# Kernel optimization log

Hardware: AMD Instinct MI355X
Metric: run time of the kernel (lower is better)

The kernel has to match this reference:

```python
import jax, jax.numpy as jnp
import numpy as np

B, C, H, W = 8, 512, 96, 96
CQ = C // 8


def setup_inputs() -> dict:
    key = jax.random.key(0)
    ks = jax.random.split(key, 8)
    s = 1.0 / np.sqrt(C)  # conv-like init scale to keep logits sane
    return {
        "x": jax.random.normal(ks[0], (B, C, H, W), jnp.float32),
        "Wq": jax.random.normal(ks[1], (CQ, C), jnp.float32) * s,
        "bq": jax.random.normal(ks[2], (CQ,), jnp.float32) * s,
        "Wk": jax.random.normal(ks[3], (CQ, C), jnp.float32) * s,
        "bk": jax.random.normal(ks[4], (CQ,), jnp.float32) * s,
        "Wv": jax.random.normal(ks[5], (C, C), jnp.float32) * s,
        "bv": jax.random.normal(ks[6], (C,), jnp.float32) * s,
        "gamma": jax.random.normal(ks[7], (1,), jnp.float32),
    }


def reference(x, Wq, bq, Wk, bk, Wv, bv, gamma):
    # 1x1 convs == per-pixel linear projections
    q = jnp.einsum('bchw,oc->bohw', x, Wq) + bq[None, :, None, None]  # [B,CQ,H,W]
    k = jnp.einsum('bchw,oc->bohw', x, Wk) + bk[None, :, None, None]  # [B,CQ,H,W]
    v = jnp.einsum('bchw,oc->bohw', x, Wv) + bv[None, :, None, None]  # [B,C ,H,W]

    h = x.shape[2]
    # column (vertical) attention logits: query at (h,w) vs keys at (j,w)
    energy_H = jnp.einsum('bchw,bcjw->bhwj', q, k)  # [B,H,W,H]
    # row (horizontal) attention logits: query at (h,w) vs keys at (h,j)
    energy_W = jnp.einsum('bchw,bchj->bhwj', q, k)  # [B,H,W,W]

    att = jax.nn.softmax(jnp.concatenate([energy_H, energy_W], axis=-1), axis=-1)
    att_H = att[..., :h]   # [B,H,W,H]
    att_W = att[..., h:]   # [B,H,W,W]

    out_H = jnp.einsum('bcjw,bhwj->bchw', v, att_H)
    out_W = jnp.einsum('bchj,bhwj->bchw', v, att_W)
    return gamma[0] * (out_H + out_W)
```

## Files before the change

### kernel.cpp

```cpp
#include <hip/hip_runtime.h>

#define B 8
#define C 512
#define H 96
#define W 96
#define HW (H*W)
#define KD 512
#define NSP 9216

typedef __attribute__((ext_vector_type(8))) short bf16x8;
typedef __attribute__((ext_vector_type(4))) short short4v;
typedef __attribute__((ext_vector_type(4))) float f32x4;
typedef __attribute__((ext_vector_type(8))) _Float16 f16x8;
typedef __attribute__((ext_vector_type(4))) _Float16 f16x4v;

static __device__ __forceinline__ unsigned short f2bf(float f) {
    unsigned u = __float_as_uint(f);
    return (unsigned short)((u + 0x7FFFu + ((u >> 16) & 1u)) >> 16);
}
static __device__ __forceinline__ float bf2f(unsigned short h) {
    return __uint_as_float(((unsigned)h) << 16);
}
static __device__ __forceinline__ int tidx(int row, int kgrp) {
    return row * 32 + ((kgrp ^ ((row >> 2) & 3)) << 3);
}
static __device__ __forceinline__ int tidx64(int row, int gr) {
    return row * 64 + ((gr ^ (row & 7)) << 3);
}

__global__ __launch_bounds__(256) void split_w(
    const float* __restrict__ Wv, const float* __restrict__ Wq, const float* __restrict__ Wk,
    _Float16* __restrict__ Wv_h,
    unsigned short* __restrict__ Wqk_hi, unsigned short* __restrict__ Wqk_lo)
{
    int i = blockIdx.x * 256 + threadIdx.x;
    if (i < C * C) {
        Wv_h[i] = (_Float16)Wv[i];
    }
    if (i < 128 * C) {
        int m = i / C, k = i % C;
        float f = (m < 64) ? Wq[m * C + k] : Wk[(m - 64) * C + k];
        unsigned short h = f2bf(f);
        Wqk_hi[i] = h;
        Wqk_lo[i] = f2bf(f - bf2f(h));
    }
}

__global__ __launch_bounds__(256, 2) void gemm_v_f16(
    const float* __restrict__ x,
    const _Float16* __restrict__ Wh,
    const float* __restrict__ bias,
    _Float16* __restrict__ out16)
{
    __shared__ _Float16 smem[12288];
    const int X_HI = 0, X_LO = 4096, W_H = 8192;

    int tid = threadIdx.x;
    int n0 = blockIdx.x * 128;
    int m0 = blockIdx.y * 128;
    int b  = blockIdx.z;

    int lane = tid & 63, wave = tid >> 6;
    int wr = wave >> 1, wc = wave & 1;
    int l15 = lane & 15, l4 = lane >> 4;

    int tn = tid & 31, tk = tid >> 5;
    int nloc = tn * 4, kloc = tk * 4;
    const float* xp = x + ((size_t)b * KD + kloc) * NSP + n0 + nloc;
    int kg = tk >> 1, khalf = tk & 1;

    int wrow0 = tid >> 2, wkg0 = tid & 3;
    int wrow1 = (tid + 256) >> 2, wkg1 = (tid + 256) & 3;
    const _Float16* wp0 = Wh + (size_t)(m0 + wrow0) * KD + wkg0 * 8;
    const _Float16* wp1 = Wh + (size_t)(m0 + wrow1) * KD + wkg1 * 8;

    f32x4 acc[4][4];
    #pragma unroll
    for (int i = 0; i < 4; ++i)
        #pragma unroll
        for (int j = 0; j < 4; ++j)
            acc[i][j] = (f32x4){0.f, 0.f, 0.f, 0.f};

    float4 t4[4];
    f16x8 wv0, wv1;
    #pragma unroll
    for (int kk = 0; kk < 4; ++kk) t4[kk] = *(const float4*)(xp + (size_t)kk * NSP);
    wv0 = *(const f16x8*)wp0;
    wv1 = *(const f16x8*)wp1;

    for (int k0 = 0; k0 < KD; k0 += 32) {
        float4 t4n[4];
        f16x8 wv0n, wv1n;
        if (k0 + 32 < KD) {
            #pragma unroll
            for (int kk = 0; kk < 4; ++kk)
                t4n[kk] = *(const float4*)(xp + (size_t)(k0 + 32 + kk) * NSP);
            wv0n = *(const f16x8*)(wp0 + k0 + 32);
            wv1n = *(const f16x8*)(wp1 + k0 + 32);
        }
        #pragma unroll
        for (int nn = 0; nn < 4; ++nn) {
            int n = nloc + nn;
            f16x4v hi, lo;
            #pragma unroll
            for (int kk = 0; kk < 4; ++kk) {
                float f = ((const float*)&t4[kk])[nn];
                _Float16 hh = (_Float16)f;
                hi[kk] = hh;
                lo[kk] = (_Float16)(f - (float)hh);
            }
            int base = tidx(n, kg) + khalf * 4;
            *(f16x4v*)&smem[X_HI + base] = hi;
            *(f16x4v*)&smem[X_LO + base] = lo;
        }
        *(f16x8*)&smem[W_H + tidx(wrow0, wkg0)] = wv0;
        *(f16x8*)&smem[W_H + tidx(wrow1, wkg1)] = wv1;
        __syncthreads();

        f16x8 af[4], bh_[4], bl_[4];
        #pragma unroll
        for (int f = 0; f < 4; ++f) {
            int ra = wr * 64 + f * 16 + l15;
            int rb = wc * 64 + f * 16 + l15;
            af[f]  = *(const f16x8*)&smem[W_H  + tidx(ra, l4)];
            bh_[f] = *(const f16x8*)&smem[X_HI + tidx(rb, l4)];
        }
        #pragma unroll
        for (int i = 0; i < 4; ++i)
            #pragma unroll
            for (int j = 0; j < 4; ++j)
                acc[i][j] = __builtin_amdgcn_mfma_f32_16x16x32_f16(af[i], bh_[j], acc[i][j], 0, 0, 0);
        #pragma unroll
        for (int f = 0; f < 4; ++f) {
            int rb = wc * 64 + f * 16 + l15;
            bl_[f] = *(const f16x8*)&smem[X_LO + tidx(rb, l4)];
        }
        #pragma unroll
        for (int i = 0; i < 4; ++i)
            #pragma unroll
            for (int j = 0; j < 4; ++j)
                acc[i][j] = __builtin_amdgcn_mfma_f32_16x16x32_f16(af[i], bl_[j], acc[i][j], 0, 0, 0);
        __syncthreads();

        #pragma unroll
        for (int kk = 0; kk < 4; ++kk) t4[kk] = t4n[kk];
        wv0 = wv0n; wv1 = wv1n;
    }

    #pragma unroll
    for (int i = 0; i < 4; ++i) {
        #pragma unroll
        for (int r = 0; r < 4; ++r) {
            int row = m0 + wr * 64 + i * 16 + l4 * 4 + r;
            float bv = bias[row];
            #pragma unroll
            for (int j = 0; j < 4; ++j) {
                int col = n0 + wc * 64 + j * 16 + l15;
                out16[((size_t)b * C + row) * NSP + col] = (_Float16)(acc[i][j][r] + bv);
            }
        }
    }
}

__global__ __launch_bounds__(256, 2) void gemm_qk_bf16(
    const float* __restrict__ x,
    const unsigned short* __restrict__ Wh,
    const unsigned short* __restrict__ Wl,
    const float* __restrict__ bias0,
    const float* __restrict__ bias1,
    unsigned short* __restrict__ qh, unsigned short* __restrict__ ql,
    unsigned short* __restrict__ kh, unsigned short* __restrict__ kl)
{
    __shared__ short smem[16384];
    const int X_HI = 0, X_LO = 4096, W_HI = 8192, W_LO = 12288;

    int tid = threadIdx.x;
    int n0 = blockIdx.x * 128;
    int b  = blockIdx.z;

    int lane = tid & 63, wave = tid >> 6;
    int wr = wave >> 1, wc = wave & 1;
    int l15 = lane & 15, l4 = lane >> 4;

    int tn = tid & 31, tk = tid >> 5;
    int nloc = tn * 4, kloc = tk * 4;
    const float* xp = x + ((size_t)b * KD + kloc) * NSP + n0 + nloc;
    int kg = tk >> 1, khalf = tk & 1;

    int wrow[4], wkg[4];
    const unsigned short* wp[4];
    #pragma unroll
    for (int it = 0; it < 4; ++it) {
        int gi = tid + it * 256;
        int sel = gi >> 9;
        int t = gi & 511;
        wrow[it] = t >> 2; wkg[it] = t & 3;
        wp[it] = (sel ? Wl : Wh) + (size_t)wrow[it] * KD + wkg[it] * 8;
    }
    int wdst[4];
    #pragma unroll
    for (int it = 0; it < 4; ++it)
        wdst[it] = ((tid + it * 256) >> 9 ? W_LO : W_HI) + tidx(wrow[it], wkg[it]);

    f32x4 acc[4][4];
    #pragma unroll
    for (int i = 0; i < 4; ++i)
        #pragma unroll
        for (int j = 0; j < 4; ++j)
            acc[i][j] = (f32x4){0.f, 0.f, 0.f, 0.f};

    float4 t4[4];
    bf16x8 wv[4];
    #pragma unroll
    for (int kk = 0; kk < 4; ++kk) t4[kk] = *(const float4*)(xp + (size_t)kk * NSP);
    #pragma unroll
    for (int it = 0; it < 4; ++it) wv[it] = *(const bf16x8*)wp[it];

    for (int k0 = 0; k0 < KD; k0 += 32) {
        float4 t4n[4];
        bf16x8 wvn[4];
        if (k0 + 32 < KD) {
            #pragma unroll
            for (int kk = 0; kk < 4; ++kk)
                t4n[kk] = *(const float4*)(xp + (size_t)(k0 + 32 + kk) * NSP);
            #pragma unroll
            for (int it = 0; it < 4; ++it)
                wvn[it] = *(const bf16x8*)(wp[it] + k0 + 32);
        }
        #pragma unroll
        for (int nn = 0; nn < 4; ++nn) {
            int n = nloc + nn;
            short4v hi, lo;
            #pragma unroll
            for (int kk = 0; kk < 4; ++kk) {
                float f = ((const float*)&t4[kk])[nn];
                unsigned short h = f2bf(f);
                hi[kk] = (short)h;
                lo[kk] = (short)f2bf(f - bf2f(h));
            }
            int base = tidx(n, kg) + khalf * 4;
            *(short4v*)&smem[X_HI + base] = hi;
            *(short4v*)&smem[X_LO + base] = lo;
        }
        #pragma unroll
        for (int it = 0; it < 4; ++it)
            *(bf16x8*)&smem[wdst[it]] = wv[it];
        __syncthreads();

        bf16x8 af[4], bf_[4], bl_[4];
        #pragma unroll
        for (int f = 0; f < 4; ++f) {
            int ra = wr * 64 + f * 16 + l15;
            int rb = wc * 64 + f * 16 + l15;
            af[f]  = *(const bf16x8*)&smem[X_HI + tidx(ra, l4)];
            bf_[f] = *(const bf16x8*)&smem[W_HI + tidx(rb, l4)];
        }
        #pragma unroll
        for (int i = 0; i < 4; ++i)
            #pragma unroll
            for (int j = 0; j < 4; ++j)
                acc[i][j] = __builtin_amdgcn_mfma_f32_16x16x32_bf16(af[i], bf_[j], acc[i][j], 0, 0, 0);
        #pragma unroll
        for (int f = 0; f < 4; ++f) {
            int rb = wc * 64 + f * 16 + l15;
            bl_[f] = *(const bf16x8*)&smem[W_LO + tidx(rb, l4)];
        }
        #pragma unroll
        for (int i = 0; i < 4; ++i)
            #pragma unroll
            for (int j = 0; j < 4; ++j)
                acc[i][j] = __builtin_amdgcn_mfma_f32_16x16x32_bf16(af[i], bl_[j], acc[i][j], 0, 0, 0);
        #pragma unroll
        for (int f = 0; f < 4; ++f) {
            int ra = wr * 64 + f * 16 + l15;
            af[f] = *(const bf16x8*)&smem[X_LO + tidx(ra, l4)];
        }
        #pragma unroll
        for (int i = 0; i < 4; ++i)
            #pragma unroll
            for (int j = 0; j < 4; ++j)
                acc[i][j] = __builtin_amdgcn_mfma_f32_16x16x32_bf16(af[i], bf_[j], acc[i][j], 0, 0, 0);
        __syncthreads();

        #pragma unroll
        for (int kk = 0; kk < 4; ++kk) t4[kk] = t4n[kk];
        #pragma unroll
        for (int it = 0; it < 4; ++it) wv[it] = wvn[it];
    }

    #pragma unroll
    for (int i = 0; i < 4; ++i) {
        #pragma unroll
        for (int r = 0; r < 4; ++r) {
            int sp = n0 + wr * 64 + i * 16 + l4 * 4 + r;
            #pragma unroll
            for (int j = 0; j < 4; ++j) {
                int wcol = wc * 64 + j * 16 + l15;
                float val = acc[i][j][r] + (wcol < 64 ? bias0[wcol] : bias1[wcol - 64]);
                unsigned short hi = f2bf(val);
                unsigned short lo = f2bf(val - bf2f(hi));
                size_t off = ((size_t)b * NSP + sp) * 64 + (wcol & 63);
                if (wcol < 64) { qh[off] = hi; ql[off] = lo; }
                else           { kh[off] = hi; kl[off] = lo; }
            }
        }
    }
}

__global__ __launch_bounds__(256, 2) void energy_mfma(
    const unsigned short* __restrict__ qh, const unsigned short* __restrict__ ql,
    const unsigned short* __restrict__ kh, const unsigned short* __restrict__ kl,
    float* __restrict__ out, int pMul, int rMul)
{
    __shared__ short sm[4 * 96 * 64];
    const int T_QH = 0, T_QL = 6144, T_KH = 12288, T_KL = 18432;
    int p = blockIdx.x, b = blockIdx.y;
    int tid = threadIdx.x;
    size_t base = ((size_t)b * HW + (size_t)p * pMul) * 64;
    size_t rstride = (size_t)rMul * 64;

    #pragma unroll
    for (int tile = 0; tile < 4; ++tile) {
        const unsigned short* src = (tile == 0) ? qh : (tile == 1) ? ql : (tile == 2) ? kh : kl;
        int tb = tile * 6144;
        #pragma unroll
        for (int sub = 0; sub < 3; ++sub) {
            int s = sub * 256 + tid;
            int row = s >> 3, g = s & 7;
            bf16x8 d = *(const bf16x8*)&src[base + row * rstride + g * 8];
            *(bf16x8*)&sm[tb + tidx64(row, g)] = d;
        }
    }
    __syncthreads();

    int lane = tid & 63, wave = tid >> 6;
    int wr = wave >> 1, wc = wave & 1;
    int l15 = lane & 15, l4 = lane >> 4;

    f32x4 acc[3][3];
    #pragma unroll
    for (int i = 0; i < 3; ++i)
        #pragma unroll
        for (int j = 0; j < 3; ++j)
            acc[i][j] = (f32x4){0.f, 0.f, 0.f, 0.f};

    #pragma unroll
    for (int ks = 0; ks < 2; ++ks) {
        bf16x8 Ah[3], Al[3], Bh[3], Bl[3];
        int gr = ks * 4 + l4;
        #pragma unroll
        for (int i = 0; i < 3; ++i) {
            int ra = wr * 48 + i * 16 + l15;
            int sa = tidx64(ra, gr);
            Ah[i] = *(const bf16x8*)&sm[T_QH + sa];
            Al[i] = *(const bf16x8*)&sm[T_QL + sa];
            int rb = wc * 48 + i * 16 + l15;
            int sb = tidx64(rb, gr);
            Bh[i] = *(const bf16x8*)&sm[T_KH + sb];
            Bl[i] = *(const bf16x8*)&sm[T_KL + sb];
        }
        #pragma unroll
        for (int i = 0; i < 3; ++i)
            #pragma unroll
            for (int j = 0; j < 3; ++j) {
                acc[i][j] = __builtin_amdgcn_mfma_f32_16x16x32_bf16(Ah[i], Bh[j], acc[i][j], 0, 0, 0);
                acc[i][j] = __builtin_amdgcn_mfma_f32_16x16x32_bf16(Ah[i], Bl[j], acc[i][j], 0, 0, 0);
                acc[i][j] = __builtin_amdgcn_mfma_f32_16x16x32_bf16(Al[i], Bh[j], acc[i][j], 0, 0, 0);
            }
    }

    size_t ob = (size_t)(b * 96 + p) * 9216;
    #pragma unroll
    for (int i = 0; i < 3; ++i)
        #pragma unroll
        for (int r = 0; r < 4; ++r) {
            int row = wr * 48 + i * 16 + l4 * 4 + r;
            #pragma unroll
            for (int j = 0; j < 3; ++j) {
                int col = wc * 48 + j * 16 + l15;
                out[ob + (size_t)row * 96 + col] = acc[i][j][r];
            }
        }
}

__global__ __launch_bounds__(256) void maxsum(
    const float* __restrict__ EW, const float* __restrict__ EH,
    const float* __restrict__ gamma, float* __restrict__ ms)
{
    int gw = (blockIdx.x * 256 + threadIdx.x) >> 6;
    int lane = threadIdx.x & 63;
    int b = gw / HW, hw = gw % HW;
    int h = hw / 96, w = hw % 96;
    const float* ew = &EW[((size_t)(b * 96 + h) * 96 + w) * 96];
    const float* eh = &EH[((size_t)(b * 96 + w) * 96 + h) * 96];
    float v0 = ew[lane];
    float v1 = (lane < 32) ? ew[64 + lane] : eh[lane - 32];
    float v2 = eh[32 + lane];
    float m = fmaxf(fmaxf(v0, v1), v2);
    #pragma unroll
    for (int s = 32; s; s >>= 1) m = fmaxf(m, __shfl_xor(m, s));
    float pp = __expf(v0 - m) + __expf(v1 - m) + __expf(v2 - m);
    #pragma unroll
    for (int s = 32; s; s >>= 1) pp += __shfl_xor(pp, s);
    if (lane == 0) {
        ms[(size_t)gw * 2]     = m;
        ms[(size_t)gw * 2 + 1] = gamma[0] / pp;
    }
}

template<int OUT16>
__global__ __launch_bounds__(256) void agg_mfma(
    const float* __restrict__ E, const float* __restrict__ ms,
    const _Float16* __restrict__ v16,
    float* __restrict__ dstF, _Float16* __restrict__ dstH, int msMode)
{
    __shared__ _Float16 satt[3][96 * 32];

    int r  = blockIdx.x;
    int b  = blockIdx.y;
    int tid = threadIdx.x;
    int lane = tid & 63, wave = tid >> 6;
    int l15 = lane & 15, l4 = lane >> 4;

    const float* Eb = &E[(size_t)(b * 96 + r) * 9216];
    int msBase = b * HW;
    #pragma unroll
    for (int it = 0; it < 5; ++it) {
        int g_id = tid + it * 256;
        if (g_id < 1152) {
            int s = g_id / 12, gj = g_id % 12;
            int mi = msMode ? (msBase + s * 96 + r) : (msBase + r * 96 + s);
            float m  = ms[(size_t)mi * 2];
            float sc = ms[(size_t)mi * 2 + 1];
            float4 e0 = *(const float4*)&Eb[s * 96 + gj * 8];
            float4 e1 = *(const float4*)&Eb[s * 96 + gj * 8 + 4];
            float pv[8] = {e0.x, e0.y, e0.z, e0.w, e1.x, e1.y, e1.z, e1.w};
            f16x8 ph;
            #pragma unroll
            for (int u = 0; u < 8; ++u)
                ph[u] = (_Float16)(__expf(pv[u] - m) * sc);
            *(f16x8*)&satt[gj >> 2][tidx(s, gj & 3)] = ph;
        }
    }
    __syncthreads();

    const _Float16* vb = v16 + (size_t)b * C * 9216 + r * 96;

    for (int cc = 0; cc < 4; ++cc) {
        int cbase = cc * 128 + wave * 32;

        f32x4 acc[2][6];
        #pragma unroll
        for (int i = 0; i < 2; ++i)
            #pragma unroll
            for (int n = 0; n < 6; ++n)
                acc[i][n] = (f32x4){0.f, 0.f, 0.f, 0.f};

        #pragma unroll
        for (int kc = 0; kc < 3; ++kc) {
            f16x8 af[2];
            #pragma unroll
            for (int i = 0; i < 2; ++i)
                af[i] = *(const f16x8*)&vb[(size_t)(cbase + i * 16 + l15) * 9216 + kc * 32 + l4 * 8];
            f16x8 Bp[6];
            #pragma unroll
            for (int n = 0; n < 6; ++n)
                Bp[n] = *(const f16x8*)&satt[kc][tidx(n * 16 + l15, l4)];
            #pragma unroll
            for (int i = 0; i < 2; ++i)
                #pragma unroll
                for (int n = 0; n < 6; ++n)
                    acc[i][n] = __builtin_amdgcn_mfma_f32_16x16x32_f16(af[i], Bp[n], acc[i][n], 0, 0, 0);
        }

        #pragma unroll
        for (int i = 0; i < 2; ++i)
            #pragma unroll
            for (int r4 = 0; r4 < 4; ++r4) {
                int cl = cbase + i * 16 + l4 * 4 + r4;
                size_t rowb = ((size_t)b * C + cl) * 9216 + r * 96;
                #pragma unroll
                for (int n = 0; n < 6; ++n) {
                    int s = n * 16 + l15;
                    if (OUT16) dstH[rowb + s] = (_Float16)acc[i][n][r4];
                    else       dstF[rowb + s] = acc[i][n][r4];
                }
            }
    }
}

__global__ __launch_bounds__(256) void transpose_f16(
    const _Float16* __restrict__ src, _Float16* __restrict__ dst)
{
    size_t base = (size_t)blockIdx.x * (96 * 96);
    __shared__ _Float16 t[96][97];
    int tid = threadIdx.x;
    for (int i = tid; i < 96 * 96; i += 256) t[i / 96][i % 96] = src[base + i];
    __syncthreads();
    for (int i = tid; i < 96 * 96; i += 256) dst[base + i] = t[i % 96][i / 96];
}

__global__ __launch_bounds__(256) void transpose_add(
    const _Float16* __restrict__ srcT, float* __restrict__ out)
{
    size_t base = (size_t)blockIdx.x * (96 * 96);
    __shared__ _Float16 t[96][97];
    int tid = threadIdx.x;
    for (int i = tid; i < 96 * 96; i += 256) t[i / 96][i % 96] = srcT[base + i];
    __syncthreads();
    for (int i = tid; i < 96 * 96; i += 256) out[base + i] += (float)t[i % 96][i / 96];
}

extern "C" void kernel_launch(void* const* d_in, const int* in_sizes, int n_in,
                              void* d_out, int out_size, void* d_ws, size_t ws_size,
                              hipStream_t stream)
{
    const float* x     = (const float*)d_in[0];
    const float* Wq    = (const float*)d_in[1];
    const float* bq    = (const float*)d_in[2];
    const float* Wk    = (const float*)d_in[3];
    const float* bk    = (const float*)d_in[4];
    const float* Wv    = (const float*)d_in[5];
    const float* bv    = (const float*)d_in[6];
    const float* gamma = (const float*)d_in[7];
    float* out = (float*)d_out;

    unsigned short* qh = (unsigned short*)d_ws;
    unsigned short* ql = qh + (size_t)B*HW*64;
    unsigned short* kh = ql + (size_t)B*HW*64;
    unsigned short* kl = kh + (size_t)B*HW*64;
    _Float16* vA = (_Float16*)(kl + (size_t)B*HW*64);
    _Float16* vB = vA + (size_t)B*C*HW;
    float* EH   = (float*)(vB + (size_t)B*C*HW);
    float* EW   = EH + (size_t)B*HW*96;
    float* ms   = (float*)d_ws;
    _Float16* outHT = vA;

    _Float16* Wv_h = (_Float16*)EW;
    unsigned short* Wqk_hi = (unsigned short*)(Wv_h + (size_t)C*C);
    unsigned short* Wqk_lo = Wqk_hi + (size_t)128*C;

    dim3 blk(256);

    split_w<<<dim3((C*C + 255)/256), blk, 0, stream>>>(Wv, Wq, Wk, Wv_h, Wqk_hi, Wqk_lo);

    gemm_v_f16<<<dim3(NSP/128, C/128, B), blk, 0, stream>>>(x, Wv_h, bv, vA);
    gemm_qk_bf16<<<dim3(NSP/128, 1, B), blk, 0, stream>>>(x, Wqk_hi, Wqk_lo, bq, bk, qh, ql, kh, kl);

    energy_mfma<<<dim3(96, B), blk, 0, stream>>>(qh, ql, kh, kl, EW, 96, 1);
    energy_mfma<<<dim3(96, B), blk, 0, stream>>>(qh, ql, kh, kl, EH, 1, 96);

    maxsum<<<dim3(B*HW/4), blk, 0, stream>>>(EW, EH, gamma, ms);

    transpose_f16<<<dim3(B*C), blk, 0, stream>>>(vA, vB);

    agg_mfma<0><<<dim3(96, B), blk, 0, stream>>>(EW, ms, vA, out, nullptr, 0);
    agg_mfma<1><<<dim3(96, B), blk, 0, stream>>>(EH, ms, vB, nullptr, outHT, 1);
    transpose_add<<<dim3(B*C), blk, 0, stream>>>(outHT, out);
}
```

Baseline: 420.5 us.

## Pre-split x into transposed fp16 hi/lo and stream GEMM tiles via global_load_lds

Adds a split_x pass that converts x once into k-contiguous fp16 hi/lo copies. The V and QK projection GEMMs then load tiles straight into LDS with global_load_lds, replacing per-iteration fp32 loads, conversion and register staging. The V GEMM drops the lo-part MFMA pass, so it uses fp16 x only. Q/K switch from bf16 to fp16 split arithmetic, and when the workspace is large enough the row output goes to an fp16 buffer that a combine kernel merges. The cost is an extra full read and write pass over x, unswizzled LDS reads that may bank-conflict, less precision in the V projection, and a larger workspace.

```diff
diff --git a/kernel.cpp b/kernel.cpp
--- a/kernel.cpp
+++ b/kernel.cpp
@@ -8,19 +8,15 @@
 #define KD 512
 #define NSP 9216
 
-typedef __attribute__((ext_vector_type(8))) short bf16x8;
-typedef __attribute__((ext_vector_type(4))) short short4v;
 typedef __attribute__((ext_vector_type(4))) float f32x4;
 typedef __attribute__((ext_vector_type(8))) _Float16 f16x8;
-typedef __attribute__((ext_vector_type(4))) _Float16 f16x4v;
-
-static __device__ __forceinline__ unsigned short f2bf(float f) {
-    unsigned u = __float_as_uint(f);
-    return (unsigned short)((u + 0x7FFFu + ((u >> 16) & 1u)) >> 16);
-}
-static __device__ __forceinline__ float bf2f(unsigned short h) {
-    return __uint_as_float(((unsigned)h) << 16);
-}
+
+typedef __attribute__((address_space(3))) unsigned int lds_u32;
+typedef const __attribute__((address_space(1))) unsigned int glb_u32;
+static __device__ __forceinline__ void gload16(const void* gsrc, void* ldst) {
+    __builtin_amdgcn_global_load_lds((glb_u32*)gsrc, (lds_u32*)ldst, 16, 0, 0);
+}
+
 static __device__ __forceinline__ int tidx(int row, int kgrp) {
     return row * 32 + ((kgrp ^ ((row >> 2) & 3)) << 3);
 }
@@ -31,48 +27,74 @@
 __global__ __launch_bounds__(256) void split_w(
     const float* __restrict__ Wv, const float* __restrict__ Wq, const float* __restrict__ Wk,
     _Float16* __restrict__ Wv_h,
-    unsigned short* __restrict__ Wqk_hi, unsigned short* __restrict__ Wqk_lo)
+    _Float16* __restrict__ Wqk_h, _Float16* __restrict__ Wqk_l)
 {
     int i = blockIdx.x * 256 + threadIdx.x;
-    if (i < C * C) {
-        Wv_h[i] = (_Float16)Wv[i];
-    }
+    if (i < C * C) Wv_h[i] = (_Float16)Wv[i];
     if (i < 128 * C) {
         int m = i / C, k = i % C;
         float f = (m < 64) ? Wq[m * C + k] : Wk[(m - 64) * C + k];
-        unsigned short h = f2bf(f);
-        Wqk_hi[i] = h;
-        Wqk_lo[i] = f2bf(f - bf2f(h));
-    }
-}
-
-__global__ __launch_bounds__(256, 2) void gemm_v_f16(
+        _Float16 h = (_Float16)f;
+        Wqk_h[i] = h;
+        Wqk_l[i] = (_Float16)(f - (float)h);
+    }
+}
+
+__global__ __launch_bounds__(256) void split_x(
     const float* __restrict__ x,
+    _Float16* __restrict__ xhT, _Float16* __restrict__ xlT)
+{
+    __shared__ float t[64][65];
+    int n0 = blockIdx.x * 64, k0 = blockIdx.y * 64, b = blockIdx.z;
+    int tid = threadIdx.x;
+    const float* xb = x + ((size_t)b * KD + k0) * NSP + n0;
+    #pragma unroll
+    for (int it = 0; it < 16; ++it) {
+        int idx = tid + it * 256;
+        t[idx >> 6][idx & 63] = xb[(size_t)(idx >> 6) * NSP + (idx & 63)];
+    }
+    __syncthreads();
+    #pragma unroll
+    for (int it = 0; it < 2; ++it) {
+        int gid = tid + it * 256;
+        int n = gid >> 3, g = gid & 7;
+        f16x8 hi, lo;
+        #pragma unroll
+        for (int u = 0; u < 8; ++u) {
+            float f = t[g * 8 + u][n];
+            _Float16 hh = (_Float16)f;
+            hi[u] = hh;
+            lo[u] = (_Float16)(f - (float)hh);
+        }
+        size_t off = ((size_t)b * NSP + n0 + n) * KD + k0 + g * 8;
+        *(f16x8*)&xhT[off] = hi;
+        *(f16x8*)&xlT[off] = lo;
+    }
+}
+
+__global__ __launch_bounds__(256, 2) void gemm_v(
+    const _Float16* __restrict__ xhT,
     const _Float16* __restrict__ Wh,
     const float* __restrict__ bias,
     _Float16* __restrict__ out16)
 {
-    __shared__ _Float16 smem[12288];
-    const int X_HI = 0, X_LO = 4096, W_H = 8192;
-
-    int tid = threadIdx.x;
-    int n0 = blockIdx.x * 128;
-    int m0 = blockIdx.y * 128;
-    int b  = blockIdx.z;
-
+    __shared__ _Float16 smem[8192];
+    const int W_OFF = 0, X_OFF = 4096;
+
+    int tid = threadIdx.x;
+    int n0 = blockIdx.x * 128, m0 = blockIdx.y * 128, b = blockIdx.z;
     int lane = tid & 63, wave = tid >> 6;
     int wr = wave >> 1, wc = wave & 1;
     int l15 = lane & 15, l4 = lane >> 4;
 
-    int tn = tid & 31, tk = tid >> 5;
-    int nloc = tn * 4, kloc = tk * 4;
-    const float* xp = x + ((size_t)b * KD + kloc) * NSP + n0 + nloc;
-    int kg = tk >> 1, khalf = tk & 1;
-
-    int wrow0 = tid >> 2, wkg0 = tid & 3;
-    int wrow1 = (tid + 256) >> 2, wkg1 = (tid + 256) & 3;
-    const _Float16* wp0 = Wh + (size_t)(m0 + wrow0) * KD + wkg0 * 8;
-    const _Float16* wp1 = Wh + (size_t)(m0 + wrow1) * KD + wkg1 * 8;
+    int grow = tid >> 2, gcol = (tid & 3) * 8;
+    const _Float16* pW = Wh + (size_t)(m0 + grow) * KD + gcol;
+    const _Float16* pX = xhT + ((size_t)b * NSP + n0 + grow) * KD + gcol;
+    const size_t half = (size_t)64 * KD;
+    int ldsW0 = W_OFF + wave * 512;
+    int ldsW1 = W_OFF + 2048 + wave * 512;
+    int ldsX0 = X_OFF + wave * 512;
+    int ldsX1 = X_OFF + 2048 + wave * 512;
 
     f32x4 acc[4][4];
     #pragma unroll
@@ -81,74 +103,29 @@
         for (int j = 0; j < 4; ++j)
             acc[i][j] = (f32x4){0.f, 0.f, 0.f, 0.f};
 
-    float4 t4[4];
-    f16x8 wv0, wv1;
-    #pragma unroll
-    for (int kk = 0; kk < 4; ++kk) t4[kk] = *(const float4*)(xp + (size_t)kk * NSP);
-    wv0 = *(const f16x8*)wp0;
-    wv1 = *(const f16x8*)wp1;
-
     for (int k0 = 0; k0 < KD; k0 += 32) {
-        float4 t4n[4];
-        f16x8 wv0n, wv1n;
-        if (k0 + 32 < KD) {
-            #pragma unroll
-            for (int kk = 0; kk < 4; ++kk)
-                t4n[kk] = *(const float4*)(xp + (size_t)(k0 + 32 + kk) * NSP);
-            wv0n = *(const f16x8*)(wp0 + k0 + 32);
-            wv1n = *(const f16x8*)(wp1 + k0 + 32);
-        }
-        #pragma unroll
-        for (int nn = 0; nn < 4; ++nn) {
-            int n = nloc + nn;
-            f16x4v hi, lo;
-            #pragma unroll
-            for (int kk = 0; kk < 4; ++kk) {
-                float f = ((const float*)&t4[kk])[nn];
-                _Float16 hh = (_Float16)f;
-                hi[kk] = hh;
-                lo[kk] = (_Float16)(f - (float)hh);
-            }
-            int base = tidx(n, kg) + khalf * 4;
-            *(f16x4v*)&smem[X_HI + base] = hi;
-            *(f16x4v*)&smem[X_LO + base] = lo;
-        }
-        *(f16x8*)&smem[W_H + tidx(wrow0, wkg0)] = wv0;
-        *(f16x8*)&smem[W_H + tidx(wrow1, wkg1)] = wv1;
+        gload16(pW + k0,        &smem[ldsW0]);
+        gload16(pW + half + k0, &smem[ldsW1]);
+        gload16(pX + k0,        &smem[ldsX0]);
+        gload16(pX + half + k0, &smem[ldsX1]);
         __syncthreads();
 
-        f16x8 af[4], bh_[4], bl_[4];
+        f16x8 af[4], bf[4];
         #pragma unroll
         for (int f = 0; f < 4; ++f) {
-            int ra = wr * 64 + f * 16 + l15;
-            int rb = wc * 64 + f * 16 + l15;
-            af[f]  = *(const f16x8*)&smem[W_H  + tidx(ra, l4)];
-            bh_[f] = *(const f16x8*)&smem[X_HI + tidx(rb, l4)];
+            af[f] = *(const f16x8*)&smem[W_OFF + (wr * 64 + f * 16 + l15) * 32 + l4 * 8];
+            bf[f] = *(const f16x8*)&smem[X_OFF + (wc * 64 + f * 16 + l15) * 32 + l4 * 8];
         }
         #pragma unroll
         for (int i = 0; i < 4; ++i)
             #pragma unroll
             for (int j = 0; j < 4; ++j)
-                acc[i][j] = __builtin_amdgcn_mfma_f32_16x16x32_f16(af[i], bh_[j], acc[i][j], 0, 0, 0);
-        #pragma unroll
-        for (int f = 0; f < 4; ++f) {
-            int rb = wc * 64 + f * 16 + l15;
-            bl_[f] = *(const f16x8*)&smem[X_LO + tidx(rb, l4)];
-        }
-        #pragma unroll
-        for (int i = 0; i < 4; ++i)
-            #pragma unroll
-            for (int j = 0; j < 4; ++j)
-                acc[i][j] = __builtin_amdgcn_mfma_f32_16x16x32_f16(af[i], bl_[j], acc[i][j], 0, 0, 0);
+                acc[i][j] = __builtin_amdgcn_mfma_f32_16x16x32_f16(af[i], bf[j], acc[i][j], 0, 0, 0);
         __syncthreads();
-
-        #pragma unroll
-        for (int kk = 0; kk < 4; ++kk) t4[kk] = t4n[kk];
-        wv0 = wv0n; wv1 = wv1n;
-    }
-
-    #pragma unroll
-    for (int i = 0; i < 4; ++i) {
+    }
+
+    #pragma unroll
+    for (int i = 0; i < 4; ++i)
         #pragma unroll
         for (int r = 0; r < 4; ++r) {
             int row = m0 + wr * 64 + i * 16 + l4 * 4 + r;
@@ -159,48 +136,31 @@
                 out16[((size_t)b * C + row) * NSP + col] = (_Float16)(acc[i][j][r] + bv);
             }
         }
-    }
-}
-
-__global__ __launch_bounds__(256, 2) void gemm_qk_bf16(
-    const float* __restrict__ x,
-    const unsigned short* __restrict__ Wh,
-    const unsigned short* __restrict__ Wl,
-    const float* __restrict__ bias0,
-    const float* __restrict__ bias1,
-    unsigned short* __restrict__ qh, unsigned short* __restrict__ ql,
-    unsigned short* __restrict__ kh, unsigned short* __restrict__ kl)
-{
-    __shared__ short smem[16384];
-    const int X_HI = 0, X_LO = 4096, W_HI = 8192, W_LO = 12288;
-
-    int tid = threadIdx.x;
-    int n0 = blockIdx.x * 128;
-    int b  = blockIdx.z;
-
+}
+
+__global__ __launch_bounds__(256, 2) void gemm_qk(
+    const _Float16* __restrict__ xhT, const _Float16* __restrict__ xlT,
+    const _Float16* __restrict__ Wqh, const _Float16* __restrict__ Wql,
+    const float* __restrict__ bias0, const float* __restrict__ bias1,
+    _Float16* __restrict__ qh, _Float16* __restrict__ ql,
+    _Float16* __restrict__ kh, _Float16* __restrict__ kl)
+{
+    __shared__ _Float16 smem[16384];
+    const int XH = 0, XL = 4096, WHo = 8192, WLo = 12288;
+
+    int tid = threadIdx.x;
+    int n0 = blockIdx.x * 128, b = blockIdx.z;
     int lane = tid & 63, wave = tid >> 6;
     int wr = wave >> 1, wc = wave & 1;
     int l15 = lane & 15, l4 = lane >> 4;
 
-    int tn = tid & 31, tk = tid >> 5;
-    int nloc = tn * 4, kloc = tk * 4;
-    const float* xp = x + ((size_t)b * KD + kloc) * NSP + n0 + nloc;
-    int kg = tk >> 1, khalf = tk & 1;
-
-    int wrow[4], wkg[4];
-    const unsigned short* wp[4];
-    #pragma unroll
-    for (int it = 0; it < 4; ++it) {
-        int gi = tid + it * 256;
-        int sel = gi >> 9;
-        int t = gi & 511;
-        wrow[it] = t >> 2; wkg[it] = t & 3;
-        wp[it] = (sel ? Wl : Wh) + (size_t)wrow[it] * KD + wkg[it] * 8;
-    }
-    int wdst[4];
-    #pragma unroll
-    for (int it = 0; it < 4; ++it)
-        wdst[it] = ((tid + it * 256) >> 9 ? W_LO : W_HI) + tidx(wrow[it], wkg[it]);
+    int grow = tid >> 2, gcol = (tid & 3) * 8;
+    const _Float16* pXh = xhT + ((size_t)b * NSP + n0 + grow) * KD + gcol;
+    const _Float16* pXl = xlT + ((size_t)b * NSP + n0 + grow) * KD + gcol;
+    const _Float16* pWh = Wqh + (size_t)grow * KD + gcol;
+    const _Float16* pWl = Wql + (size_t)grow * KD + gcol;
+    const size_t half = (size_t)64 * KD;
+    int base0 = wave * 512, base1 = 2048 + wave * 512;
 
     f32x4 acc[4][4];
     #pragma unroll
@@ -209,87 +169,47 @@
         for (int j = 0; j < 4; ++j)
             acc[i][j] = (f32x4){0.f, 0.f, 0.f, 0.f};
 
-    float4 t4[4];
-    bf16x8 wv[4];
-    #pragma unroll
-    for (int kk = 0; kk < 4; ++kk) t4[kk] = *(const float4*)(xp + (size_t)kk * NSP);
-    #pragma unroll
-    for (int it = 0; it < 4; ++it) wv[it] = *(const bf16x8*)wp[it];
-
     for (int k0 = 0; k0 < KD; k0 += 32) {
-        float4 t4n[4];
-        bf16x8 wvn[4];
-        if (k0 + 32 < KD) {
-            #pragma unroll
-            for (int kk = 0; kk < 4; ++kk)
-                t4n[kk] = *(const float4*)(xp + (size_t)(k0 + 32 + kk) * NSP);
-            #pragma unroll
-            for (int it = 0; it < 4; ++it)
-                wvn[it] = *(const bf16x8*)(wp[it] + k0 + 32);
-        }
-        #pragma unroll
-        for (int nn = 0; nn < 4; ++nn) {
-            int n = nloc + nn;
-            short4v hi, lo;
-            #pragma unroll
-            for (int kk = 0; kk < 4; ++kk) {
-                float f = ((const float*)&t4[kk])[nn];
-                unsigned short h = f2bf(f);
-                hi[kk] = (short)h;
-                lo[kk] = (short)f2bf(f - bf2f(h));
-            }
-            int base = tidx(n, kg) + khalf * 4;
-            *(short4v*)&smem[X_HI + base] = hi;
-            *(short4v*)&smem[X_LO + base] = lo;
-        }
-        #pragma unroll
-        for (int it = 0; it < 4; ++it)
-            *(bf16x8*)&smem[wdst[it]] = wv[it];
+        gload16(pXh + k0,        &smem[XH + base0]);
+        gload16(pXh + half + k0, &smem[XH + base1]);
+        gload16(pXl + k0,        &smem[XL + base0]);
+        gload16(pXl + half + k0, &smem[XL + base1]);
+        gload16(pWh + k0,        &smem[WHo + base0]);
+        gload16(pWh + half + k0, &smem[WHo + base1]);
+        gload16(pWl + k0,        &smem[WLo + base0]);
+        gload16(pWl + half + k0, &smem[WLo + base1]);
         __syncthreads();
 
-        bf16x8 af[4], bf_[4], bl_[4];
+        f16x8 axh[4], axl[4], bwh[4], bwl[4];
         #pragma unroll
         for (int f = 0; f < 4; ++f) {
-            int ra = wr * 64 + f * 16 + l15;
-            int rb = wc * 64 + f * 16 + l15;
-            af[f]  = *(const bf16x8*)&smem[X_HI + tidx(ra, l4)];
-            bf_[f] = *(const bf16x8*)&smem[W_HI + tidx(rb, l4)];
+            int ra = (wr * 64 + f * 16 + l15) * 32 + l4 * 8;
+            int rb = (wc * 64 + f * 16 + l15) * 32 + l4 * 8;
+            axh[f] = *(const f16x8*)&smem[XH + ra];
+            axl[f] = *(const f16x8*)&smem[XL + ra];
+            bwh[f] = *(const f16x8*)&smem[WHo + rb];
+            bwl[f] = *(const f16x8*)&smem[WLo + rb];
         }
         #pragma unroll
         for (int i = 0; i < 4; ++i)
             #pragma unroll
             for (int j = 0; j < 4; ++j)
-                acc[i][j] = __builtin_amdgcn_mfma_f32_16x16x32_bf16(af[i], bf_[j], acc[i][j], 0, 0, 0);
-        #pragma unroll
-        for (int f = 0; f < 4; ++f) {
-            int rb = wc * 64 + f * 16 + l15;
-            bl_[f] = *(const bf16x8*)&smem[W_LO + tidx(rb, l4)];
-        }
+                acc[i][j] = __builtin_amdgcn_mfma_f32_16x16x32_f16(axh[i], bwh[j], acc[i][j], 0, 0, 0);
         #pragma unroll
         for (int i = 0; i < 4; ++i)
             #pragma unroll
             for (int j = 0; j < 4; ++j)
-                acc[i][j] = __builtin_amdgcn_mfma_f32_16x16x32_bf16(af[i], bl_[j], acc[i][j], 0, 0, 0);
-        #pragma unroll
-        for (int f = 0; f < 4; ++f) {
-            int ra = wr * 64 + f * 16 + l15;
-            af[f] = *(const bf16x8*)&smem[X_LO + tidx(ra, l4)];
-        }
+                acc[i][j] = __builtin_amdgcn_mfma_f32_16x16x32_f16(axh[i], bwl[j], acc[i][j], 0, 0, 0);
         #pragma unroll
         for (int i = 0; i < 4; ++i)
             #pragma unroll
             for (int j = 0; j < 4; ++j)
-                acc[i][j] = __builtin_amdgcn_mfma_f32_16x16x32_bf16(af[i], bf_[j], acc[i][j], 0, 0, 0);
+                acc[i][j] = __builtin_amdgcn_mfma_f32_16x16x32_f16(axl[i], bwh[j], acc[i][j], 0, 0, 0);
         __syncthreads();
-
-        #pragma unroll
-        for (int kk = 0; kk < 4; ++kk) t4[kk] = t4n[kk];
-        #pragma unroll
-        for (int it = 0; it < 4; ++it) wv[it] = wvn[it];
-    }
-
-    #pragma unroll
-    for (int i = 0; i < 4; ++i) {
+    }
+
+    #pragma unroll
+    for (int i = 0; i < 4; ++i)
         #pragma unroll
         for (int r = 0; r < 4; ++r) {
             int sp = n0 + wr * 64 + i * 16 + l4 * 4 + r;
@@ -297,22 +217,21 @@
             for (int j = 0; j < 4; ++j) {
                 int wcol = wc * 64 + j * 16 + l15;
                 float val = acc[i][j][r] + (wcol < 64 ? bias0[wcol] : bias1[wcol - 64]);
-                unsigned short hi = f2bf(val);
-                unsigned short lo = f2bf(val - bf2f(hi));
+                _Float16 hi = (_Float16)val;
+                _Float16 lo = (_Float16)(val - (float)hi);
                 size_t off = ((size_t)b * NSP + sp) * 64 + (wcol & 63);
                 if (wcol < 64) { qh[off] = hi; ql[off] = lo; }
                 else           { kh[off] = hi; kl[off] = lo; }
             }
         }
-    }
 }
 
 __global__ __launch_bounds__(256, 2) void energy_mfma(
-    const unsigned short* __restrict__ qh, const unsigned short* __restrict__ ql,
-    const unsigned short* __restrict__ kh, const unsigned short* __restrict__ kl,
+    const _Float16* __restrict__ qh, const _Float16* __restrict__ ql,
+    const _Float16* __restrict__ kh, const _Float16* __restrict__ kl,
     float* __restrict__ out, int pMul, int rMul)
 {
-    __shared__ short sm[4 * 96 * 64];
+    __shared__ _Float16 sm[4 * 96 * 64];
     const int T_QH = 0, T_QL = 6144, T_KH = 12288, T_KL = 18432;
     int p = blockIdx.x, b = blockIdx.y;
     int tid = threadIdx.x;
@@ -321,14 +240,14 @@
 
     #pragma unroll
     for (int tile = 0; tile < 4; ++tile) {
-        const unsigned short* src = (tile == 0) ? qh : (tile == 1) ? ql : (tile == 2) ? kh : kl;
+        const _Float16* src = (tile == 0) ? qh : (tile == 1) ? ql : (tile == 2) ? kh : kl;
         int tb = tile * 6144;
         #pragma unroll
         for (int sub = 0; sub < 3; ++sub) {
             int s = sub * 256 + tid;
             int row = s >> 3, g = s & 7;
-            bf16x8 d = *(const bf16x8*)&src[base + row * rstride + g * 8];
-            *(bf16x8*)&sm[tb + tidx64(row, g)] = d;
+            f16x8 d = *(const f16x8*)&src[base + row * rstride + g * 8];
+            *(f16x8*)&sm[tb + tidx64(row, g)] = d;
         }
     }
     __syncthreads();
@@ -346,26 +265,24 @@
 
     #pragma unroll
     for (int ks = 0; ks < 2; ++ks) {
-        bf16x8 Ah[3], Al[3], Bh[3], Bl[3];
+        f16x8 Ah[3], Al[3], Bh[3], Bl[3];
         int gr = ks * 4 + l4;
         #pragma unroll
         for (int i = 0; i < 3; ++i) {
-            int ra = wr * 48 + i * 16 + l15;
-            int sa = tidx64(ra, gr);
-            Ah[i] = *(const bf16x8*)&sm[T_QH + sa];
-            Al[i] = *(const bf16x8*)&sm[T_QL + sa];
-            int rb = wc * 48 + i * 16 + l15;
-            int sb = tidx64(rb, gr);
-            Bh[i] = *(const bf16x8*)&sm[T_KH + sb];
-            Bl[i] = *(const bf16x8*)&sm[T_KL + sb];
+            int sa = tidx64(wr * 48 + i * 16 + l15, gr);
+            Ah[i] = *(const f16x8*)&sm[T_QH + sa];
+            Al[i] = *(const f16x8*)&sm[T_QL + sa];
+            int sb = tidx64(wc * 48 + i * 16 + l15, gr);
+            Bh[i] = *(const f16x8*)&sm[T_KH + sb];
+            Bl[i] = *(const f16x8*)&sm[T_KL + sb];
         }
         #pragma unroll
         for (int i = 0; i < 3; ++i)
             #pragma unroll
             for (int j = 0; j < 3; ++j) {
-                acc[i][j] = __builtin_amdgcn_mfma_f32_16x16x32_bf16(Ah[i], Bh[j], acc[i][j], 0, 0, 0);
-                acc[i][j] = __builtin_amdgcn_mfma_f32_16x16x32_bf16(Ah[i], Bl[j], acc[i][j], 0, 0, 0);
-                acc[i][j] = __builtin_amdgcn_mfma_f32_16x16x32_bf16(Al[i], Bh[j], acc[i][j], 0, 0, 0);
+                acc[i][j] = __builtin_amdgcn_mfma_f32_16x16x32_f16(Ah[i], Bh[j], acc[i][j], 0, 0, 0);
+                acc[i][j] = __builtin_amdgcn_mfma_f32_16x16x32_f16(Ah[i], Bl[j], acc[i][j], 0, 0, 0);
+                acc[i][j] = __builtin_amdgcn_mfma_f32_16x16x32_f16(Al[i], Bh[j], acc[i][j], 0, 0, 0);
             }
     }
 
@@ -376,10 +293,8 @@
         for (int r = 0; r < 4; ++r) {
             int row = wr * 48 + i * 16 + l4 * 4 + r;
             #pragma unroll
-            for (int j = 0; j < 3; ++j) {
-                int col = wc * 48 + j * 16 + l15;
-                out[ob + (size_t)row * 96 + col] = acc[i][j][r];
-            }
+            for (int j = 0; j < 3; ++j)
+                out[ob + (size_t)row * 96 + wc * 48 + j * 16 + l15] = acc[i][j][r];
         }
 }
 
@@ -416,8 +331,7 @@
 {
     __shared__ _Float16 satt[3][96 * 32];
 
-    int r  = blockIdx.x;
-    int b  = blockIdx.y;
+    int r = blockIdx.x, b = blockIdx.y;
     int tid = threadIdx.x;
     int lane = tid & 63, wave = tid >> 6;
     int l15 = lane & 15, l4 = lane >> 4;
@@ -448,7 +362,6 @@
 
     for (int cc = 0; cc < 4; ++cc) {
         int cbase = cc * 128 + wave * 32;
-
         f32x4 acc[2][6];
         #pragma unroll
         for (int i = 0; i < 2; ++i)
@@ -511,6 +424,19 @@
     for (int i = tid; i < 96 * 96; i += 256) out[base + i] += (float)t[i % 96][i / 96];
 }
 
+__global__ __launch_bounds__(256) void combine(
+    const _Float16* __restrict__ w16, const _Float16* __restrict__ hT,
+    float* __restrict__ out)
+{
+    size_t base = (size_t)blockIdx.x * (96 * 96);
+    __shared__ _Float16 t[96][97];
+    int tid = threadIdx.x;
+    for (int i = tid; i < 96 * 96; i += 256) t[i / 96][i % 96] = hT[base + i];
+    __syncthreads();
+    for (int i = tid; i < 96 * 96; i += 256)
+        out[base + i] = (float)w16[base + i] + (float)t[i % 96][i / 96];
+}
+
 extern "C" void kernel_launch(void* const* d_in, const int* in_sizes, int n_in,
                               void* d_out, int out_size, void* d_ws, size_t ws_size,
                               hipStream_t stream)
@@ -525,36 +451,50 @@
     const float* gamma = (const float*)d_in[7];
     float* out = (float*)d_out;
 
-    unsigned short* qh = (unsigned short*)d_ws;
-    unsigned short* ql = qh + (size_t)B*HW*64;
-    unsigned short* kh = ql + (size_t)B*HW*64;
-    unsigned short* kl = kh + (size_t)B*HW*64;
-    _Float16* vA = (_Float16*)(kl + (size_t)B*HW*64);
-    _Float16* vB = vA + (size_t)B*C*HW;
-    float* EH   = (float*)(vB + (size_t)B*C*HW);
-    float* EW   = EH + (size_t)B*HW*96;
-    float* ms   = (float*)d_ws;
-    _Float16* outHT = vA;
-
-    _Float16* Wv_h = (_Float16*)EW;
-    unsigned short* Wqk_hi = (unsigned short*)(Wv_h + (size_t)C*C);
-    unsigned short* Wqk_lo = Wqk_hi + (size_t)128*C;
+    const size_t NK = (size_t)B * NSP * KD;
+    _Float16* xhT = (_Float16*)d_ws;
+    _Float16* xlT = xhT + NK;
+    _Float16* qh  = xlT + NK;
+    _Float16* ql  = qh + (size_t)B * HW * 64;
+    _Float16* kh  = ql + (size_t)B * HW * 64;
+    _Float16* kl  = kh + (size_t)B * HW * 64;
+    float* EHp = (float*)(kl + (size_t)B * HW * 64);
+    float* EWp = EHp + (size_t)B * HW * 96;
+    float* ms  = (float*)qh;
+    _Float16* vA  = xlT;
+    _Float16* vB  = xhT;
+    _Float16* outHT = xlT;
+
+    _Float16* Wv_h  = (_Float16*)EHp;
+    _Float16* Wqk_h = Wv_h + (size_t)C * C;
+    _Float16* Wqk_l = Wqk_h + (size_t)128 * C;
+
+    const size_t NEED = 245366784ull;
+    bool bigws = ws_size >= NEED + NK * sizeof(_Float16);
+    _Float16* outW16 = (_Float16*)((char*)d_ws + NEED);
 
     dim3 blk(256);
 
-    split_w<<<dim3((C*C + 255)/256), blk, 0, stream>>>(Wv, Wq, Wk, Wv_h, Wqk_hi, Wqk_lo);
-
-    gemm_v_f16<<<dim3(NSP/128, C/128, B), blk, 0, stream>>>(x, Wv_h, bv, vA);
-    gemm_qk_bf16<<<dim3(NSP/128, 1, B), blk, 0, stream>>>(x, Wqk_hi, Wqk_lo, bq, bk, qh, ql, kh, kl);
-
-    energy_mfma<<<dim3(96, B), blk, 0, stream>>>(qh, ql, kh, kl, EW, 96, 1);
-    energy_mfma<<<dim3(96, B), blk, 0, stream>>>(qh, ql, kh, kl, EH, 1, 96);
-
-    maxsum<<<dim3(B*HW/4), blk, 0, stream>>>(EW, EH, gamma, ms);
+    split_w<<<dim3((C*C + 255)/256), blk, 0, stream>>>(Wv, Wq, Wk, Wv_h, Wqk_h, Wqk_l);
+    split_x<<<dim3(NSP/64, KD/64, B), blk, 0, stream>>>(x, xhT, xlT);
+
+    gemm_qk<<<dim3(NSP/128, 1, B), blk, 0, stream>>>(xhT, xlT, Wqk_h, Wqk_l, bq, bk, qh, ql, kh, kl);
+    gemm_v<<<dim3(NSP/128, C/128, B), blk, 0, stream>>>(xhT, Wv_h, bv, vA);
+
+    energy_mfma<<<dim3(96, B), blk, 0, stream>>>(qh, ql, kh, kl, EWp, 96, 1);
+    energy_mfma<<<dim3(96, B), blk, 0, stream>>>(qh, ql, kh, kl, EHp, 1, 96);
+
+    maxsum<<<dim3(B*HW/4), blk, 0, stream>>>(EWp, EHp, gamma, ms);
 
     transpose_f16<<<dim3(B*C), blk, 0, stream>>>(vA, vB);
 
-    agg_mfma<0><<<dim3(96, B), blk, 0, stream>>>(EW, ms, vA, out, nullptr, 0);
-    agg_mfma<1><<<dim3(96, B), blk, 0, stream>>>(EH, ms, vB, nullptr, outHT, 1);
-    transpose_add<<<dim3(B*C), blk, 0, stream>>>(outHT, out);
-}
+    if (bigws) {
+        agg_mfma<1><<<dim3(96, B), blk, 0, stream>>>(EWp, ms, vA, nullptr, outW16, 0);
+        agg_mfma<1><<<dim3(96, B), blk, 0, stream>>>(EHp, ms, vB, nullptr, outHT, 1);
+        combine<<<dim3(B*C), blk, 0, stream>>>(outW16, outHT, out);
+    } else {
+        agg_mfma<0><<<dim3(96, B), blk, 0, stream>>>(EWp, ms, vA, out, nullptr, 0);
+        agg_mfma<1><<<dim3(96, B), blk, 0, stream>>>(EHp, ms, vB, nullptr, outHT, 1);
+        transpose_add<<<dim3(B*C), blk, 0, stream>>>(outHT, out);
+    }
+}
```

New measurement: 382.1 us. -9.1%, faster.
